# Kernel optimization log

Hardware: AMD Instinct MI355X
Metric: run time of the kernel (lower is better)

Reference implementation:

```python
import jax, jax.numpy as jnp
import numpy as np

N_NODE = 4096
N_FEA_IN = 128
N_FEA_OUT = 128


def setup_inputs() -> dict:
    key = jax.random.key(0)
    k_x, k_a, k_w, k_att = jax.random.split(key, 4)
    stdv_w = 1.0 / np.sqrt(N_FEA_OUT)       # torch reset: 1/sqrt(W.size(1))
    stdv_a = 1.0 / np.sqrt(2 * N_FEA_OUT)   # a is [1, 2*n_fea_out]
    X = jax.random.normal(k_x, (N_NODE, N_FEA_IN), dtype=jnp.float32)
    A = jax.random.uniform(k_a, (N_NODE, N_NODE), dtype=jnp.float32)  # dense weighted adjacency
    W = jax.random.uniform(k_w, (N_FEA_IN, N_FEA_OUT), minval=-stdv_w, maxval=stdv_w, dtype=jnp.float32)
    a = jax.random.uniform(k_att, (1, 2 * N_FEA_OUT), minval=-stdv_a, maxval=stdv_a, dtype=jnp.float32)
    return {"X": X, "A": A, "W": W, "a": a}


def reference(X, A, W, a):
    # XW: [N, F_out]
    XW = jnp.matmul(X, W)
    f = W.shape[1]
    # Z[i,j] = concat(XW[j], XW[i]); Z @ a.T decomposes into two rank-1 broadcasts:
    s_col = jnp.matmul(XW, a[0, :f])   # depends on column index j
    s_row = jnp.matmul(XW, a[0, f:])   # depends on row index i
    Z1 = jax.nn.leaky_relu(s_row[:, None] + s_col[None, :], negative_slope=0.01)  # [N, N]
    den = jnp.exp(Z1)                  # [N, N]
    num = jnp.matmul(A, den)           # numerator[i,j] = sum_k A[i,k] * den[k,j]
    # vectorized replacement of the Python double loop: att = den/num where num != 0
    att = jnp.where(num != 0, den / jnp.where(num != 0, num, 1.0), 0.0)
    H = jnp.matmul(A, jnp.matmul(att, XW))
    return H
```

## Files before the change

kernel.cpp:

```cpp
#include <hip/hip_runtime.h>
#include <hip/hip_bf16.h>
#include <stdint.h>

#define NN 4096
#define NF 128
#define NSPLIT 16

using f32x4  = __attribute__((ext_vector_type(4))) float;
using bf16x8 = __attribute__((ext_vector_type(8))) __bf16;
using u16x8  = __attribute__((ext_vector_type(8))) uint16_t;

__device__ __forceinline__ uint16_t f2b(float f) {
    union { float f; uint32_t u; } v; v.f = f;
    uint32_t r = v.u + 0x7FFFu + ((v.u >> 16) & 1u);
    return (uint16_t)(r >> 16);
}

__device__ __forceinline__ float b2f(uint16_t u) {
    union { uint32_t u; float f; } v; v.u = ((uint32_t)u) << 16;
    return v.f;
}

__device__ __forceinline__ void gld_lds16(const void* g, void* l) {
    __builtin_amdgcn_global_load_lds(
        (const __attribute__((address_space(1))) uint32_t*)g,
        (__attribute__((address_space(3))) uint32_t*)l,
        16, 0, 0);
}

__global__ void xw_kernel(const float* __restrict__ X, const float* __restrict__ W,
                          const float* __restrict__ a,
                          uint16_t* __restrict__ XWT,
                          float* __restrict__ s_col, float* __restrict__ s_row) {
    __shared__ float xs[NF];
    __shared__ float red[4];
    const int i = blockIdx.x, f = threadIdx.x;
    xs[f] = X[i * NF + f];
    __syncthreads();
    float acc = 0.f;
    #pragma unroll 8
    for (int k = 0; k < NF; ++k) acc += xs[k] * W[k * NF + f];
    XWT[(size_t)f * NN + i] = f2b(acc);
    float sc = acc * a[f];
    float sr = acc * a[NF + f];
    #pragma unroll
    for (int off = 32; off; off >>= 1) {
        sc += __shfl_down(sc, off);
        sr += __shfl_down(sr, off);
    }
    if ((f & 63) == 0) { red[f >> 6] = sc; red[2 + (f >> 6)] = sr; }
    __syncthreads();
    if (f == 0) {
        s_col[i] = red[0] + red[1];
        s_row[i] = red[2] + red[3];
    }
}

__global__ __launch_bounds__(256) void prep_kernel(
    const float* __restrict__ s_row, const float* __restrict__ s_col,
    int* __restrict__ ks, float* __restrict__ w1s, float* __restrict__ w2s,
    float4* __restrict__ rec) {
    __shared__ __align__(16) float sr[NN];
    const int t = threadIdx.x;
    #pragma unroll
    for (int c = 0; c < 16; ++c) sr[t + c * 256] = s_row[t + c * 256];
    __syncthreads();
    const bool isC = blockIdx.x >= 128;
    const int tgt = (blockIdx.x & 127) * 32 + (t >> 3);
    const int sub = t & 7;
    const float4* sr4 = (const float4*)sr;
    int cnt = 0;
    if (!isC) {
        const float s = sr[tgt];
        #pragma unroll 4
        for (int q = 0; q < 128; ++q) {
            const int k4 = q * 8 + sub;
            float4 v = sr4[k4];
            const int kb = k4 * 4;
            cnt += (v.x < s) | ((v.x == s) & (kb + 0 < tgt));
            cnt += (v.y < s) | ((v.y == s) & (kb + 1 < tgt));
            cnt += (v.z < s) | ((v.z == s) & (kb + 2 < tgt));
            cnt += (v.w < s) | ((v.w == s) & (kb + 3 < tgt));
        }
    } else {
        const float th = -s_col[tgt];
        #pragma unroll 4
        for (int q = 0; q < 128; ++q) {
            float4 v = sr4[q * 8 + sub];
            cnt += (v.x <= th) + (v.y <= th) + (v.z <= th) + (v.w <= th);
        }
    }
    cnt += __shfl_down(cnt, 4);
    cnt += __shfl_down(cnt, 2);
    cnt += __shfl_down(cnt, 1);
    if (sub == 0) {
        if (!isC) {
            const float s = sr[tgt];
            ks[cnt]  = tgt;
            w1s[cnt] = __expf(s);
            w2s[cnt] = __expf(0.01f * s);
        } else {
            const float sc = s_col[tgt];
            rec[tgt] = (float4){__int_as_float(cnt), __expf(sc), __expf(0.01f * sc), sc};
        }
    }
}

#define PB(b) ((b) + (((b) >> 4) << 1))

__global__ __launch_bounds__(512, 8) void row_kernel(
    const float* __restrict__ A,
    const float* __restrict__ s_row,
    const int* __restrict__ ks, const float* __restrict__ w1s, const float* __restrict__ w2s,
    const float4* __restrict__ rec,
    uint16_t* __restrict__ Ab, uint16_t* __restrict__ att) {
    __shared__ __align__(16) float rowA[NN];
    __shared__ __align__(16) uint16_t S1[4640];
    __shared__ __align__(16) uint16_t S2[4640];
    __shared__ float wtot[2][8];
    const int i = blockIdx.x, t = threadIdx.x;

    {
        const float4* Ar = (const float4*)(A + (size_t)i * NN);
        ushort4* Abr = (ushort4*)(Ab + (size_t)i * NN);
        #pragma unroll
        for (int c = 0; c < 2; ++c) {
            float4 v = Ar[t + c * 512];
            ((float4*)rowA)[t + c * 512] = v;
            ushort4 o; o.x = f2b(v.x); o.y = f2b(v.y); o.z = f2b(v.z); o.w = f2b(v.w);
            Abr[t + c * 512] = o;
        }
    }
    __syncthreads();

    float l1[8], l2[8];
    {
        const int4*   k4 = (const int4*)ks;
        const float4* a4 = (const float4*)w1s;
        const float4* b4 = (const float4*)w2s;
        float run1 = 0.f, run2 = 0.f;
        #pragma unroll
        for (int g = 0; g < 2; ++g) {
            int4   kk = k4[2 * t + g];
            float4 wa = a4[2 * t + g];
            float4 wb = b4[2 * t + g];
            float g0 = rowA[kk.x], g1 = rowA[kk.y], g2 = rowA[kk.z], g3 = rowA[kk.w];
            run1 += g0 * wa.x; l1[4 * g + 0] = run1;  run2 += g0 * wb.x; l2[4 * g + 0] = run2;
            run1 += g1 * wa.y; l1[4 * g + 1] = run1;  run2 += g1 * wb.y; l2[4 * g + 1] = run2;
            run1 += g2 * wa.z; l1[4 * g + 2] = run1;  run2 += g2 * wb.z; l2[4 * g + 2] = run2;
            run1 += g3 * wa.w; l1[4 * g + 3] = run1;  run2 += g3 * wb.w; l2[4 * g + 3] = run2;
        }
    }
    float s1 = l1[7], s2 = l2[7];
    const int lane = t & 63, wid = t >> 6;
    #pragma unroll
    for (int off = 1; off < 64; off <<= 1) {
        float u1 = __shfl_up(s1, off);
        float u2 = __shfl_up(s2, off);
        if (lane >= off) { s1 += u1; s2 += u2; }
    }
    if (lane == 63) { wtot[0][wid] = s1; wtot[1][wid] = s2; }
    __syncthreads();

    float off1 = 0.f, off2 = 0.f, tot1 = 0.f, tot2 = 0.f;
    #pragma unroll
    for (int w = 0; w < 8; ++w) {
        const float va = wtot[0][w], vb = wtot[1][w];
        tot1 += va; tot2 += vb;
        if (w < wid) { off1 += va; off2 += vb; }
    }
    const float ex1 = off1 + s1 - l1[7];
    const float ex2 = off2 + s2 - l2[7];
    {
        uint32_t* q1 = (uint32_t*)S1;
        uint32_t* q2 = (uint32_t*)S2;
        const int qb = t * 4 + (t >> 1);
        #pragma unroll
        for (int m = 0; m < 4; ++m) {
            const float pl1 = m ? l1[2 * m - 1] : 0.f;
            const float pl2 = m ? l2[2 * m - 1] : 0.f;
            const float sa = tot1 - ex1 - pl1;
            const float sb = tot1 - ex1 - l1[2 * m];
            const float pa = ex2 + pl2;
            const float pb = ex2 + l2[2 * m];
            q1[qb + m] = (uint32_t)f2b(sa) | ((uint32_t)f2b(sb) << 16);
            q2[qb + m] = (uint32_t)f2b(pa) | ((uint32_t)f2b(pb) << 16);
        }
    }
    if (t == 511) {
        S1[PB(4096)] = 0;
        S2[PB(4096)] = f2b(tot2);
    }
    __syncthreads();

    const float sri = s_row[i];
    uint32_t* attR = (uint32_t*)(att + (size_t)i * NN);
    #pragma unroll
    for (int e = 0; e < 4; ++e) {
        const int j0 = e * 1024 + 2 * t;
        const float4 ra = rec[j0];
        const float4 rb = rec[j0 + 1];
        const int Ca = __float_as_int(ra.x);
        const int Cb = __float_as_int(rb.x);
        const float numa = ra.y * b2f(S1[PB(Ca)]) + ra.z * b2f(S2[PB(Ca)]);
        const float numb = rb.y * b2f(S1[PB(Cb)]) + rb.z * b2f(S2[PB(Cb)]);
        float za = sri + ra.w; za = za > 0.f ? za : 0.01f * za;
        float zb = sri + rb.w; zb = zb > 0.f ? zb : 0.01f * zb;
        const float dena = __expf(za);
        const float denb = __expf(zb);
        const float va = (numa != 0.f) ? dena * __builtin_amdgcn_rcpf(numa) : 0.f;
        const float vb = (numb != 0.f) ? denb * __builtin_amdgcn_rcpf(numb) : 0.f;
        attR[e * 512 + t] = (uint32_t)f2b(va) | ((uint32_t)f2b(vb) << 16);
    }
}

__device__ __forceinline__ void gemm_core(
    const uint16_t* __restrict__ Ab, const uint16_t* __restrict__ Bt,
    int bm0, int bn0, int kBeg, int kEnd, int K,
    uint16_t* As, uint16_t* Bs, f32x4 acc[4][4]) {
    const int tid  = threadIdx.x;
    const int lane = tid & 63;
    const int wid  = tid >> 6;
    const int wy   = wid >> 1, wx = wid & 1;
    const int quad = lane >> 4, l16 = lane & 15;
    const int byteoff = tid * 16;
    const int srow    = byteoff >> 6;
    const int scol    = (byteoff & 63) >> 1;

    for (int k0 = kBeg; k0 < kEnd; k0 += 32) {
        __syncthreads();
        gld_lds16(Ab + (size_t)(bm0 +      srow) * K + k0 + scol, (char*)As +        byteoff);
        gld_lds16(Ab + (size_t)(bm0 + 64 + srow) * K + k0 + scol, (char*)As + 4096 + byteoff);
        gld_lds16(Bt + (size_t)(bn0 +      srow) * K + k0 + scol, (char*)Bs +        byteoff);
        gld_lds16(Bt + (size_t)(bn0 + 64 + srow) * K + k0 + scol, (char*)Bs + 4096 + byteoff);
        __syncthreads();
        bf16x8 af[4], bf[4];
        #pragma unroll
        for (int mi = 0; mi < 4; ++mi)
            af[mi] = *(const bf16x8*)((const char*)As + ((wy * 64 + mi * 16 + l16) * 64 + quad * 16));
        #pragma unroll
        for (int ni = 0; ni < 4; ++ni)
            bf[ni] = *(const bf16x8*)((const char*)Bs + ((wx * 64 + ni * 16 + l16) * 64 + quad * 16));
        #pragma unroll
        for (int mi = 0; mi < 4; ++mi)
            #pragma unroll
            for (int ni = 0; ni < 4; ++ni)
                acc[mi][ni] = __builtin_amdgcn_mfma_f32_16x16x32_bf16(af[mi], bf[ni], acc[mi][ni], 0, 0, 0);
    }
}

__global__ __launch_bounds__(256) void gemm_splitk_kernel(
    const uint16_t* __restrict__ Ab, const uint16_t* __restrict__ Bt,
    float* __restrict__ P) {
    __shared__ __align__(16) uint16_t As[128 * 32];
    __shared__ __align__(16) uint16_t Bs[128 * 32];
    const int bm0 = blockIdx.y * 128;
    const int split = blockIdx.z;
    const int chunk = NN / NSPLIT;
    f32x4 acc[4][4];
    #pragma unroll
    for (int mi = 0; mi < 4; ++mi)
        #pragma unroll
        for (int ni = 0; ni < 4; ++ni)
            acc[mi][ni] = (f32x4){0.f, 0.f, 0.f, 0.f};

    gemm_core(Ab, Bt, bm0, 0, split * chunk, (split + 1) * chunk, NN, As, Bs, acc);

    const int lane = threadIdx.x & 63, wid = threadIdx.x >> 6;
    const int wy = wid >> 1, wx = wid & 1;
    const int quad = lane >> 4, l16 = lane & 15;
    float* Pp = P + (size_t)split * (NN * NF);
    #pragma unroll
    for (int mi = 0; mi < 4; ++mi) {
        const int i0 = bm0 + wy * 64 + mi * 16 + quad * 4;
        #pragma unroll
        for (int ni = 0; ni < 4; ++ni) {
            const int j = wx * 64 + ni * 16 + l16;
            *(f32x4*)(Pp + (size_t)j * NN + i0) = acc[mi][ni];
        }
    }
}

__global__ void reduce_t_kernel(const float* __restrict__ P, uint16_t* __restrict__ M1T) {
    int idx = blockIdx.x * 256 + threadIdx.x;
    float s = 0.f;
    #pragma unroll
    for (int sp = 0; sp < NSPLIT; ++sp) s += P[(size_t)sp * (NN * NF) + idx];
    M1T[idx] = f2b(s);
}

__global__ void reduce_out_kernel(const float* __restrict__ P, float* __restrict__ out) {
    int idx = blockIdx.x * 256 + threadIdx.x;
    float s = 0.f;
    #pragma unroll
    for (int sp = 0; sp < NSPLIT; ++sp) s += P[(size_t)sp * (NN * NF) + idx];
    int j = idx >> 12, i = idx & 4095;
    out[(size_t)i * NF + j] = s;
}

extern "C" void kernel_launch(void* const* d_in, const int* in_sizes, int n_in,
                              void* d_out, int out_size, void* d_ws, size_t ws_size,
                              hipStream_t stream) {
    (void)in_sizes; (void)n_in; (void)out_size; (void)ws_size;
    const float* X = (const float*)d_in[0];
    const float* A = (const float*)d_in[1];
    const float* W = (const float*)d_in[2];
    const float* a = (const float*)d_in[3];
    float* H = (float*)d_out;

    char* ws = (char*)d_ws;
    uint16_t* Ab  = (uint16_t*)(ws);
    uint16_t* att = (uint16_t*)(ws + ((size_t)32 << 20));
    float*    P   = (float*)   (ws + ((size_t)64 << 20));
    uint16_t* XWT = (uint16_t*)(ws + ((size_t)96 << 20));
    uint16_t* M1T = (uint16_t*)(ws + ((size_t)97 << 20));
    char* sm = ws + ((size_t)64 << 20);
    float*  s_col = (float*) (sm);
    float*  s_row = (float*) (sm + (16 << 10));
    int*    ks    = (int*)   (sm + (32 << 10));
    float*  w1s   = (float*) (sm + (48 << 10));
    float*  w2s   = (float*) (sm + (64 << 10));
    float4* rec   = (float4*)(sm + (80 << 10));

    xw_kernel<<<NN, NF, 0, stream>>>(X, W, a, XWT, s_col, s_row);
    prep_kernel<<<256, 256, 0, stream>>>(s_row, s_col, ks, w1s, w2s, rec);
    row_kernel<<<NN, 512, 0, stream>>>(A, s_row, ks, w1s, w2s, rec, Ab, att);
    gemm_splitk_kernel<<<dim3(1, 32, NSPLIT), 256, 0, stream>>>(att, XWT, P);
    reduce_t_kernel<<<(NN * NF) / 256, 256, 0, stream>>>(P, M1T);
    gemm_splitk_kernel<<<dim3(1, 32, NSPLIT), 256, 0, stream>>>(Ab, M1T, P);
    reduce_out_kernel<<<(NN * NF) / 256, 256, 0, stream>>>(P, H);
}
```

Before: 203.2 us.

## Batch XW rows, load GEMM fragments directly, vectorize and tile split-K reductions

The XW kernel now computes four rows per block so each W load is reused four times, and it writes XWT as ushort4. The split-K GEMM drops the LDS staging and barriers and loads MFMA fragments straight from global memory. The reduce_t kernel uses float4 loads. The output reduction transposes through shared memory so stores to H are coalesced. The aim is fewer redundant loads, fewer sync points and uncoalesced writes, at the cost of GEMM global loads that read only 16 bytes per row and rely on cache reuse.

After: 209.9 us. 1.03x slower.

```diff
diff --git a/kernel.cpp b/kernel.cpp
--- a/kernel.cpp
+++ b/kernel.cpp
@@ -5,6 +5,7 @@
 #define NN 4096
 #define NF 128
 #define NSPLIT 16
+#define XROWS 4
 
 using f32x4  = __attribute__((ext_vector_type(4))) float;
 using bf16x8 = __attribute__((ext_vector_type(8))) __bf16;
@@ -21,38 +22,43 @@
     return v.f;
 }
 
-__device__ __forceinline__ void gld_lds16(const void* g, void* l) {
-    __builtin_amdgcn_global_load_lds(
-        (const __attribute__((address_space(1))) uint32_t*)g,
-        (__attribute__((address_space(3))) uint32_t*)l,
-        16, 0, 0);
-}
-
-__global__ void xw_kernel(const float* __restrict__ X, const float* __restrict__ W,
-                          const float* __restrict__ a,
-                          uint16_t* __restrict__ XWT,
-                          float* __restrict__ s_col, float* __restrict__ s_row) {
-    __shared__ float xs[NF];
-    __shared__ float red[4];
-    const int i = blockIdx.x, f = threadIdx.x;
-    xs[f] = X[i * NF + f];
-    __syncthreads();
-    float acc = 0.f;
-    #pragma unroll 8
-    for (int k = 0; k < NF; ++k) acc += xs[k] * W[k * NF + f];
-    XWT[(size_t)f * NN + i] = f2b(acc);
-    float sc = acc * a[f];
-    float sr = acc * a[NF + f];
-    #pragma unroll
-    for (int off = 32; off; off >>= 1) {
-        sc += __shfl_down(sc, off);
-        sr += __shfl_down(sr, off);
-    }
-    if ((f & 63) == 0) { red[f >> 6] = sc; red[2 + (f >> 6)] = sr; }
-    __syncthreads();
-    if (f == 0) {
-        s_col[i] = red[0] + red[1];
-        s_row[i] = red[2] + red[3];
+__global__ __launch_bounds__(128) void xw_kernel(
+    const float* __restrict__ X, const float* __restrict__ W,
+    const float* __restrict__ a,
+    uint16_t* __restrict__ XWT,
+    float* __restrict__ s_col, float* __restrict__ s_row) {
+    __shared__ float xs[XROWS][NF];
+    __shared__ float red[XROWS][2][2];
+    const int i0 = blockIdx.x * XROWS, f = threadIdx.x;
+    #pragma unroll
+    for (int r = 0; r < XROWS; ++r) xs[r][f] = X[(size_t)(i0 + r) * NF + f];
+    __syncthreads();
+    float acc[XROWS] = {0.f, 0.f, 0.f, 0.f};
+    #pragma unroll 4
+    for (int k = 0; k < NF; ++k) {
+        const float w = W[k * NF + f];
+        #pragma unroll
+        for (int r = 0; r < XROWS; ++r) acc[r] += xs[r][k] * w;
+    }
+    ushort4 xo;
+    xo.x = f2b(acc[0]); xo.y = f2b(acc[1]); xo.z = f2b(acc[2]); xo.w = f2b(acc[3]);
+    *(ushort4*)(XWT + (size_t)f * NN + i0) = xo;
+    const float a1 = a[f], a2 = a[NF + f];
+    #pragma unroll
+    for (int r = 0; r < XROWS; ++r) {
+        float sc = acc[r] * a1;
+        float sr = acc[r] * a2;
+        #pragma unroll
+        for (int off = 32; off; off >>= 1) {
+            sc += __shfl_down(sc, off);
+            sr += __shfl_down(sr, off);
+        }
+        if ((f & 63) == 0) { red[r][f >> 6][0] = sc; red[r][f >> 6][1] = sr; }
+    }
+    __syncthreads();
+    if (f < XROWS) {
+        s_col[i0 + f] = red[f][0][0] + red[f][1][0];
+        s_row[i0 + f] = red[f][0][1] + red[f][1][1];
     }
 }
 
@@ -214,61 +220,43 @@
     }
 }
 
-__device__ __forceinline__ void gemm_core(
-    const uint16_t* __restrict__ Ab, const uint16_t* __restrict__ Bt,
-    int bm0, int bn0, int kBeg, int kEnd, int K,
-    uint16_t* As, uint16_t* Bs, f32x4 acc[4][4]) {
-    const int tid  = threadIdx.x;
-    const int lane = tid & 63;
-    const int wid  = tid >> 6;
-    const int wy   = wid >> 1, wx = wid & 1;
+__global__ __launch_bounds__(256) void gemm_splitk_kernel(
+    const uint16_t* __restrict__ Abt, const uint16_t* __restrict__ Bt,
+    float* __restrict__ P) {
+    const int bm0 = blockIdx.y * 128;
+    const int split = blockIdx.z;
+    const int kBeg = split * (NN / NSPLIT);
+    const int lane = threadIdx.x & 63, wid = threadIdx.x >> 6;
+    const int wy = wid >> 1, wx = wid & 1;
     const int quad = lane >> 4, l16 = lane & 15;
-    const int byteoff = tid * 16;
-    const int srow    = byteoff >> 6;
-    const int scol    = (byteoff & 63) >> 1;
-
-    for (int k0 = kBeg; k0 < kEnd; k0 += 32) {
-        __syncthreads();
-        gld_lds16(Ab + (size_t)(bm0 +      srow) * K + k0 + scol, (char*)As +        byteoff);
-        gld_lds16(Ab + (size_t)(bm0 + 64 + srow) * K + k0 + scol, (char*)As + 4096 + byteoff);
-        gld_lds16(Bt + (size_t)(bn0 +      srow) * K + k0 + scol, (char*)Bs +        byteoff);
-        gld_lds16(Bt + (size_t)(bn0 + 64 + srow) * K + k0 + scol, (char*)Bs + 4096 + byteoff);
-        __syncthreads();
+
+    f32x4 acc[4][4];
+    #pragma unroll
+    for (int mi = 0; mi < 4; ++mi)
+        #pragma unroll
+        for (int ni = 0; ni < 4; ++ni)
+            acc[mi][ni] = (f32x4){0.f, 0.f, 0.f, 0.f};
+
+    const uint16_t* Ap = Abt + (size_t)(bm0 + wy * 64 + l16) * NN + quad * 8;
+    const uint16_t* Bp = Bt  + (size_t)(wx * 64 + l16) * NN + quad * 8;
+
+    #pragma unroll 2
+    for (int kk = 0; kk < NN / NSPLIT; kk += 32) {
+        const int k0 = kBeg + kk;
         bf16x8 af[4], bf[4];
         #pragma unroll
         for (int mi = 0; mi < 4; ++mi)
-            af[mi] = *(const bf16x8*)((const char*)As + ((wy * 64 + mi * 16 + l16) * 64 + quad * 16));
+            af[mi] = *(const bf16x8*)(Ap + (size_t)(mi * 16) * NN + k0);
         #pragma unroll
         for (int ni = 0; ni < 4; ++ni)
-            bf[ni] = *(const bf16x8*)((const char*)Bs + ((wx * 64 + ni * 16 + l16) * 64 + quad * 16));
+            bf[ni] = *(const bf16x8*)(Bp + (size_t)(ni * 16) * NN + k0);
         #pragma unroll
         for (int mi = 0; mi < 4; ++mi)
             #pragma unroll
             for (int ni = 0; ni < 4; ++ni)
                 acc[mi][ni] = __builtin_amdgcn_mfma_f32_16x16x32_bf16(af[mi], bf[ni], acc[mi][ni], 0, 0, 0);
     }
-}
-
-__global__ __launch_bounds__(256) void gemm_splitk_kernel(
-    const uint16_t* __restrict__ Ab, const uint16_t* __restrict__ Bt,
-    float* __restrict__ P) {
-    __shared__ __align__(16) uint16_t As[128 * 32];
-    __shared__ __align__(16) uint16_t Bs[128 * 32];
-    const int bm0 = blockIdx.y * 128;
-    const int split = blockIdx.z;
-    const int chunk = NN / NSPLIT;
-    f32x4 acc[4][4];
-    #pragma unroll
-    for (int mi = 0; mi < 4; ++mi)
-        #pragma unroll
-        for (int ni = 0; ni < 4; ++ni)
-            acc[mi][ni] = (f32x4){0.f, 0.f, 0.f, 0.f};
-
-    gemm_core(Ab, Bt, bm0, 0, split * chunk, (split + 1) * chunk, NN, As, Bs, acc);
-
-    const int lane = threadIdx.x & 63, wid = threadIdx.x >> 6;
-    const int wy = wid >> 1, wx = wid & 1;
-    const int quad = lane >> 4, l16 = lane & 15;
+
     float* Pp = P + (size_t)split * (NN * NF);
     #pragma unroll
     for (int mi = 0; mi < 4; ++mi) {
@@ -281,21 +269,42 @@
     }
 }
 
-__global__ void reduce_t_kernel(const float* __restrict__ P, uint16_t* __restrict__ M1T) {
-    int idx = blockIdx.x * 256 + threadIdx.x;
-    float s = 0.f;
-    #pragma unroll
-    for (int sp = 0; sp < NSPLIT; ++sp) s += P[(size_t)sp * (NN * NF) + idx];
-    M1T[idx] = f2b(s);
-}
-
-__global__ void reduce_out_kernel(const float* __restrict__ P, float* __restrict__ out) {
-    int idx = blockIdx.x * 256 + threadIdx.x;
-    float s = 0.f;
-    #pragma unroll
-    for (int sp = 0; sp < NSPLIT; ++sp) s += P[(size_t)sp * (NN * NF) + idx];
-    int j = idx >> 12, i = idx & 4095;
-    out[(size_t)i * NF + j] = s;
+__global__ __launch_bounds__(256) void reduce_t_kernel(
+    const float* __restrict__ P, uint16_t* __restrict__ M1T) {
+    const int idx = (blockIdx.x * 256 + threadIdx.x) * 4;
+    f32x4 s = (f32x4){0.f, 0.f, 0.f, 0.f};
+    #pragma unroll
+    for (int sp = 0; sp < NSPLIT; ++sp)
+        s += *(const f32x4*)(P + (size_t)sp * (NN * NF) + idx);
+    ushort4 o;
+    o.x = f2b(s[0]); o.y = f2b(s[1]); o.z = f2b(s[2]); o.w = f2b(s[3]);
+    *(ushort4*)(M1T + idx) = o;
+}
+
+__global__ __launch_bounds__(256) void reduce_out_kernel(
+    const float* __restrict__ P, float* __restrict__ out) {
+    __shared__ float acc[NF][17];
+    const int i0 = blockIdx.x * 16;
+    const int t = threadIdx.x;
+    const int ii = t & 15, jb = t >> 4;
+    float local[8];
+    #pragma unroll
+    for (int jj = 0; jj < 8; ++jj) local[jj] = 0.f;
+    for (int sp = 0; sp < NSPLIT; ++sp) {
+        const float* Pp = P + (size_t)sp * (NN * NF) + i0 + ii;
+        #pragma unroll
+        for (int jj = 0; jj < 8; ++jj)
+            local[jj] += Pp[(size_t)(jb + jj * 16) * NN];
+    }
+    #pragma unroll
+    for (int jj = 0; jj < 8; ++jj) acc[jb + jj * 16][ii] = local[jj];
+    __syncthreads();
+    const int j = t & 127, rb = t >> 7;
+    #pragma unroll
+    for (int p = 0; p < 8; ++p) {
+        const int r = rb + p * 2;
+        out[(size_t)(i0 + r) * NF + j] = acc[j][r];
+    }
 }
 
 extern "C" void kernel_launch(void* const* d_in, const int* in_sizes, int n_in,
@@ -322,11 +331,11 @@
     float*  w2s   = (float*) (sm + (64 << 10));
     float4* rec   = (float4*)(sm + (80 << 10));
 
-    xw_kernel<<<NN, NF, 0, stream>>>(X, W, a, XWT, s_col, s_row);
+    xw_kernel<<<NN / XROWS, NF, 0, stream>>>(X, W, a, XWT, s_col, s_row);
     prep_kernel<<<256, 256, 0, stream>>>(s_row, s_col, ks, w1s, w2s, rec);
     row_kernel<<<NN, 512, 0, stream>>>(A, s_row, ks, w1s, w2s, rec, Ab, att);
     gemm_splitk_kernel<<<dim3(1, 32, NSPLIT), 256, 0, stream>>>(att, XWT, P);
-    reduce_t_kernel<<<(NN * NF) / 256, 256, 0, stream>>>(P, M1T);
+    reduce_t_kernel<<<(NN * NF / 4) / 256, 256, 0, stream>>>(P, M1T);
     gemm_splitk_kernel<<<dim3(1, 32, NSPLIT), 256, 0, stream>>>(Ab, M1T, P);
-    reduce_out_kernel<<<(NN * NF) / 256, 256, 0, stream>>>(P, H);
-}
+    reduce_out_kernel<<<NN / 16, 256, 0, stream>>>(P, H);
+}
```
